# Kernel optimization log

Measured on AMD Instinct MI355X. Metric: run time of the kernel, lower is better.

The kernel has to match this reference:

```python
import jax, jax.numpy as jnp
import numpy as np

N = 8192        # n_nodes
NFEAT = 512
NHID = 256
AVG_DEG = 32
K = 64          # mean_kwargs k
TEMP = 1.0      # mean_kwargs temperature


def setup_inputs() -> dict:
    key = jax.random.key(0)
    ks = jax.random.split(key, 5)
    x = jax.random.normal(ks[0], (N, NFEAT), jnp.float32)
    edge_index = jax.random.randint(ks[1], (2, N * AVG_DEG), 0, N, dtype=jnp.int64)
    W1 = jax.random.normal(ks[2], (NFEAT, NHID), jnp.float32) / np.sqrt(NFEAT)
    b1 = jnp.zeros((NHID,), jnp.float32)
    W2 = jax.random.normal(ks[3], (NHID, NHID), jnp.float32) / np.sqrt(NHID)
    b2 = jnp.zeros((NHID,), jnp.float32)
    return {"x": x, "edge_index": edge_index, "W1": W1, "b1": b1, "W2": W2, "b2": b2}


def _gcn_norm(edge_index, n, dtype):
    # PyG gcn_norm: add self-loops (weight 1), deg over col, sym normalization
    loops = jnp.arange(n, dtype=edge_index.dtype)
    row = jnp.concatenate([edge_index[0], loops])
    col = jnp.concatenate([edge_index[1], loops])
    w = jnp.ones(row.shape[0], dtype)
    deg = jnp.zeros((n,), dtype).at[col].add(w)
    dis = jnp.where(deg > 0, jax.lax.rsqrt(jnp.where(deg > 0, deg, 1.0)), 0.0)
    return row, col, dis[row] * w * dis[col]


def _soft_k_medoid(row, col, w, x):
    # soft_weighted_medoid_k_neighborhood(A, x, k=K, temperature=TEMP, with_weight_correction=True)
    n, d = x.shape
    A = jnp.zeros((n, n), x.dtype).at[row, col].add(w)   # coalesced dense adjacency
    topk_a, topk_idx = jax.lax.top_k(A, K)               # [n, K] neighbor weights / ids
    xk = x[topk_idx]                                     # [n, K, d]
    sq = jnp.sum(xk * xk, axis=-1)                       # [n, K]
    G = jnp.einsum('nkd,nld->nkl', xk, xk)               # Gram per node
    d2 = jnp.maximum(sq[:, :, None] + sq[:, None, :] - 2.0 * G, 0.0)
    pos = d2 > 0
    dist = jnp.where(pos, jnp.sqrt(jnp.where(pos, d2, 1.0)), 0.0)  # safe sqrt (grad-safe)
    # weighted sum of distances to each top-k candidate j: c[n,j] = sum_l a[n,l] * ||x_l - x_j||
    c = jnp.einsum('nl,nlj->nj', topk_a, dist)
    c = jnp.where(topk_a == 0, jnp.finfo(x.dtype).max, c)
    soft = jax.nn.softmax(-c / TEMP, axis=-1)            # [n, K]
    soft = soft * topk_a                                 # with_weight_correction
    soft = soft / jnp.sum(soft, axis=-1, keepdims=True)
    row_sum = jnp.sum(A, axis=-1)                        # preserve neighborhood mass
    return row_sum[:, None] * jnp.einsum('nk,nkd->nd', soft, xk)


def reference(x, edge_index, W1, b1, W2, b2):
    n = x.shape[0]
    row, col, w = _gcn_norm(edge_index, n, x.dtype)
    h = jax.nn.relu(_soft_k_medoid(row, col, w, x @ W1) + b1)   # gc1 + relu (dropout: eval = identity)
    return jax.nn.relu(_soft_k_medoid(row, col, w, h @ W2) + b2)  # gc2 + relu
```

## Files before the change

kernel.cpp:

```cpp
#include <hip/hip_runtime.h>

typedef _Float16 half4 __attribute__((ext_vector_type(4)));
typedef _Float16 half8 __attribute__((ext_vector_type(8)));
typedef float f32x4 __attribute__((ext_vector_type(4)));

#define NNODE 8192
#define NHID  256
#define RCAP  128
#define KCAP  64
#define GLS   72
#define SK    136

struct SmemGemm  { _Float16 sA[64][GLS]; _Float16 sB[64][GLS]; };
struct SmemDedup { int lc[2][RCAP]; float lw[2][RCAP]; unsigned char kp[2][RCAP];
                   int cw[2][2]; float rw[2][2]; };
struct SmemMedoid {
    union {
        _Float16 sh[64][SK];
        float s_red[4][288];
    };
    float s_a[64]; float s_sq[64]; float s_cpart[2][64]; float s_u[64];
    int s_cols[64]; float s_rsum;
};

__device__ __forceinline__ void gemm_body(
    char* smraw, const _Float16* __restrict__ Ahi, const _Float16* __restrict__ BT,
    _Float16* __restrict__ Chi, int K, int bm, int bn) {
    SmemGemm& sm = *(SmemGemm*)smraw;
    const int t = threadIdx.x;
    const int lane = t & 63, L15 = lane & 15, q = lane >> 4;
    const int w = t >> 6, wr = w >> 1, wc = w & 1;
    f32x4 acc[2][2];
#pragma unroll
    for (int a = 0; a < 2; ++a)
#pragma unroll
        for (int b2 = 0; b2 < 2; ++b2) acc[a][b2] = (f32x4){0.f, 0.f, 0.f, 0.f};

    for (int k0 = 0; k0 < K; k0 += 64) {
#pragma unroll
        for (int i = 0; i < 2; ++i) {
            int row = i * 32 + (t >> 3), ch = t & 7;
            *(half8*)&sm.sA[row][ch * 8] =
                *(const half8*)(Ahi + (size_t)(bm + row) * K + k0 + ch * 8);
            *(half8*)&sm.sB[row][ch * 8] =
                *(const half8*)(BT + (size_t)(bn + row) * K + k0 + ch * 8);
        }
        __syncthreads();
#pragma unroll
        for (int ks = 0; ks < 2; ++ks) {
            const int ko = ks * 32 + q * 8;
            half8 ah[2], bh[2];
#pragma unroll
            for (int tr = 0; tr < 2; ++tr)
                ah[tr] = *(const half8*)&sm.sA[32 * wr + 16 * tr + L15][ko];
#pragma unroll
            for (int tc = 0; tc < 2; ++tc)
                bh[tc] = *(const half8*)&sm.sB[32 * wc + 16 * tc + L15][ko];
#pragma unroll
            for (int tr = 0; tr < 2; ++tr)
#pragma unroll
                for (int tc = 0; tc < 2; ++tc)
                    acc[tr][tc] = __builtin_amdgcn_mfma_f32_16x16x32_f16(ah[tr], bh[tc], acc[tr][tc], 0, 0, 0);
        }
        __syncthreads();
    }
#pragma unroll
    for (int tr = 0; tr < 2; ++tr)
#pragma unroll
        for (int tc = 0; tc < 2; ++tc)
#pragma unroll
            for (int r = 0; r < 4; ++r) {
                int rowg = bm + 32 * wr + 16 * tr + q * 4 + r;
                int colg = bn + 32 * wc + 16 * tc + L15;
                Chi[(size_t)rowg * NHID + colg] = (_Float16)acc[tr][tc][r];
            }
}

__device__ __forceinline__ void dedup_body(
    char* smraw, const int* __restrict__ nbr, const int* __restrict__ rowcnt,
    const int* __restrict__ deg, int* __restrict__ cols, float* __restrict__ wout,
    float* __restrict__ rsum, int grp) {
    SmemDedup& sm = *(SmemDedup*)smraw;
    const int t = threadIdx.x;
    const int half = t >> 7, st = t & 127;
    const int wid = st >> 6, lane = t & 63;
    const int r = grp * 2 + half;
    int n = rowcnt[r]; if (n > RCAP) n = RCAP;
    if (st < n) sm.lc[half][st] = nbr[r * RCAP + st];
    __syncthreads();
    float dr = 1.f / sqrtf((float)deg[r]);
    bool keep = false; float wv = 0.f;
    if (st < n) {
        int c = sm.lc[half][st];
        int mult = 0; bool first = true;
        for (int i = 0; i < n; ++i) {
            int ci = sm.lc[half][i];
            if (ci == c) { mult++; if (i < st) first = false; }
        }
        keep = first;
        if (first) wv = (float)mult * dr * (1.f / sqrtf((float)deg[c]));
    }
    sm.kp[half][st] = keep ? 1 : 0; sm.lw[half][st] = wv;
    float rv = wv;
#pragma unroll
    for (int d = 1; d < 64; d <<= 1) rv += __shfl_xor(rv, d, 64);
    unsigned long long b = __ballot(keep);
    int pre = __popcll(b & ((1ull << lane) - 1ull));
    int cw = __popcll(b);
    if (lane == 0) { sm.cw[half][wid] = cw; sm.rw[half][wid] = rv; }
    __syncthreads();
    int total = sm.cw[half][0] + sm.cw[half][1];
    if (st == 0) rsum[r] = sm.rw[half][0] + sm.rw[half][1];
    const int base = r * KCAP;
    if (total <= KCAP) {
        int off = (wid ? sm.cw[half][0] : 0) + pre;
        if (keep) { cols[base + off] = sm.lc[half][st]; wout[base + off] = wv; }
        for (int m = total + st; m < KCAP; m += 128) { cols[base + m] = r; wout[base + m] = 0.f; }
    } else if (st == 0) {
        for (int s = 0; s < KCAP; ++s) {
            int best = -1;
            for (int i = 0; i < n; ++i) {
                if (!sm.kp[half][i]) continue;
                if (best < 0 || sm.lw[half][i] > sm.lw[half][best] ||
                    (sm.lw[half][i] == sm.lw[half][best] && sm.lc[half][i] < sm.lc[half][best])) best = i;
            }
            cols[base + s] = sm.lc[half][best]; wout[base + s] = sm.lw[half][best]; sm.kp[half][best] = 0;
        }
    }
}

__device__ __forceinline__ void medoid_core(
    SmemMedoid& sm, const _Float16* __restrict__ Xhi, const float* __restrict__ bias,
    float* __restrict__ OutF, _Float16* __restrict__ OutHi, int node, int writeH) {
    const int t = threadIdx.x;
    const int w = t >> 6, lane = t & 63;
    const int L15 = lane & 15, q = lane >> 4;
    const int wr = w >> 1, wc = w & 1;

    f32x4 acc[2][2];
#pragma unroll
    for (int a = 0; a < 2; ++a)
#pragma unroll
        for (int b = 0; b < 2; ++b) acc[a][b] = (f32x4){0.f, 0.f, 0.f, 0.f};

    const int ch = t & 15, rr = t >> 4;
    const _Float16* rbase[4];
#pragma unroll
    for (int i = 0; i < 4; ++i)
        rbase[i] = Xhi + ((size_t)sm.s_cols[i * 16 + rr] << 8) + ch * 8;

    half8 g0[4];
#pragma unroll
    for (int i = 0; i < 4; ++i) g0[i] = *(const half8*)rbase[i];
#pragma unroll
    for (int i = 0; i < 4; ++i) *(half8*)&sm.sh[i * 16 + rr][ch * 8] = g0[i];
    __syncthreads();

    half8 g1[4];
#pragma unroll
    for (int i = 0; i < 4; ++i) g1[i] = *(const half8*)(rbase[i] + 128);

#pragma unroll
    for (int ks = 0; ks < 4; ++ks) {
        const int ko = ks * 32 + q * 8;
        half8 ah[2], bh[2];
#pragma unroll
        for (int tr = 0; tr < 2; ++tr) ah[tr] = *(const half8*)&sm.sh[32 * wr + 16 * tr + L15][ko];
#pragma unroll
        for (int tc = 0; tc < 2; ++tc) bh[tc] = *(const half8*)&sm.sh[32 * wc + 16 * tc + L15][ko];
#pragma unroll
        for (int tr = 0; tr < 2; ++tr)
#pragma unroll
            for (int tc = 0; tc < 2; ++tc)
                acc[tr][tc] = __builtin_amdgcn_mfma_f32_16x16x32_f16(ah[tr], bh[tc], acc[tr][tc], 0, 0, 0);
    }
    __syncthreads();

#pragma unroll
    for (int i = 0; i < 4; ++i) *(half8*)&sm.sh[i * 16 + rr][ch * 8] = g1[i];
    __syncthreads();
#pragma unroll
    for (int ks = 0; ks < 4; ++ks) {
        const int ko = ks * 32 + q * 8;
        half8 ah[2], bh[2];
#pragma unroll
        for (int tr = 0; tr < 2; ++tr) ah[tr] = *(const half8*)&sm.sh[32 * wr + 16 * tr + L15][ko];
#pragma unroll
        for (int tc = 0; tc < 2; ++tc) bh[tc] = *(const half8*)&sm.sh[32 * wc + 16 * tc + L15][ko];
#pragma unroll
        for (int tr = 0; tr < 2; ++tr)
#pragma unroll
            for (int tc = 0; tc < 2; ++tc)
                acc[tr][tc] = __builtin_amdgcn_mfma_f32_16x16x32_f16(ah[tr], bh[tc], acc[tr][tc], 0, 0, 0);
    }

#pragma unroll
    for (int tr = 0; tr < 2; ++tr)
#pragma unroll
        for (int tc = 0; tc < 2; ++tc)
            if (32 * wr + 16 * tr == 32 * wc + 16 * tc) {
#pragma unroll
                for (int r = 0; r < 4; ++r)
                    if (L15 == q * 4 + r) sm.s_sq[32 * wr + 16 * tr + L15] = acc[tr][tc][r];
            }
    __syncthreads();

    f32x4 sq4[2], a4[2];
#pragma unroll
    for (int tr = 0; tr < 2; ++tr) {
        sq4[tr] = *(const f32x4*)&sm.s_sq[32 * wr + 16 * tr + 4 * q];
        a4[tr]  = *(const f32x4*)&sm.s_a [32 * wr + 16 * tr + 4 * q];
    }
#pragma unroll
    for (int tc = 0; tc < 2; ++tc) {
        const int colg = 32 * wc + 16 * tc + L15;
        const float sqc = sm.s_sq[colg];
        float pj = 0.f;
#pragma unroll
        for (int tr = 0; tr < 2; ++tr)
#pragma unroll
            for (int r = 0; r < 4; ++r) {
                float d2 = sq4[tr][r] + sqc - 2.f * acc[tr][tc][r];
                float dist = d2 > 0.f ? __builtin_amdgcn_sqrtf(d2) : 0.f;
                pj = fmaf(a4[tr][r], dist, pj);
            }
        pj += __shfl_xor(pj, 16, 64);
        pj += __shfl_xor(pj, 32, 64);
        if (q == 0) sm.s_cpart[wr][colg] = pj;
    }
    __syncthreads();

    if (w == 0) {
        int j = lane;
        float c = sm.s_cpart[0][j] + sm.s_cpart[1][j];
        float aj = sm.s_a[j];
        bool valid = aj > 0.f;
        float cv = valid ? c : 3.4e38f;
        float mn = cv;
#pragma unroll
        for (int d = 1; d < 64; d <<= 1) mn = fminf(mn, __shfl_xor(mn, d, 64));
        float e = valid ? __expf(mn - c) * aj : 0.f;
        float s = e;
#pragma unroll
        for (int d = 1; d < 64; d <<= 1) s += __shfl_xor(s, d, 64);
        sm.s_u[j] = e * (sm.s_rsum / s);
    }
    __syncthreads();

    const int oct = t & 31, jb = t >> 5;
    float accd[8] = {0.f, 0.f, 0.f, 0.f, 0.f, 0.f, 0.f, 0.f};
#pragma unroll
    for (int jj = 0; jj < 8; ++jj) {
        int j = jb * 8 + jj;
        float u = sm.s_u[j];
        half8 xv;
        if (oct < 16) xv = *(const half8*)(Xhi + ((size_t)sm.s_cols[j] << 8) + oct * 8);
        else          xv = *(const half8*)&sm.sh[j][(oct - 16) * 8];
#pragma unroll
        for (int e = 0; e < 8; ++e) accd[e] = fmaf(u, (float)xv[e], accd[e]);
    }
#pragma unroll
    for (int e = 0; e < 8; ++e) accd[e] += __shfl_xor(accd[e], 32, 64);
    __syncthreads();
    if (lane < 32) {
#pragma unroll
        for (int e = 0; e < 8; ++e) sm.s_red[w][9 * oct + e] = accd[e];
    }
    __syncthreads();
    const int idx = 9 * (t >> 3) + (t & 7);
    float o = sm.s_red[0][idx] + sm.s_red[1][idx] + sm.s_red[2][idx] + sm.s_red[3][idx];
    float res = fmaxf(o + bias[t], 0.f);
    size_t oi = (size_t)node * NHID + t;
    if (writeH) OutHi[oi] = (_Float16)res;
    else        OutF[oi] = res;
}

#define PREPB 512
__global__ __launch_bounds__(256) void k_prep_scatter(
    const float* __restrict__ x, _Float16* __restrict__ xh,
    const float* __restrict__ W1, _Float16* __restrict__ w1T,
    const float* __restrict__ W2, _Float16* __restrict__ w2T,
    const void* edges, int* rowcnt, int* nbr, int* deg, int E) {
    const int t = threadIdx.x;
    if ((int)blockIdx.x < PREPB) {
        const int gid = blockIdx.x * 256 + t, nthr = PREPB * 256;
        for (int i = gid; i < NNODE * 512 / 4; i += nthr) {
            float4 v = ((const float4*)x)[i];
            half4 h;
            h[0] = (_Float16)v.x; h[1] = (_Float16)v.y;
            h[2] = (_Float16)v.z; h[3] = (_Float16)v.w;
            *(half4*)&xh[4 * (size_t)i] = h;
        }
        for (int i = gid; i < 512 * NHID; i += nthr) {
            int k = i >> 8, n = i & 255;
            w1T[(size_t)n * 512 + k] = (_Float16)W1[i];
        }
        for (int i = gid; i < NHID * NHID; i += nthr) {
            int k = i >> 8, n = i & 255;
            w2T[(size_t)n * 256 + k] = (_Float16)W2[i];
        }
    } else {
        __shared__ int sflag;
        if (t < 64) {
            const long long* e = (const long long*)edges;
            long long v = e[t];
            unsigned long long bad = __ballot(v < 0 || v >= (long long)NNODE);
            if (t == 0) sflag = (bad == 0) ? 1 : 0;
        }
        __syncthreads();
        const int fl = sflag;
        int i = ((int)blockIdx.x - PREPB) * 256 + t;
        if (i >= E + NNODE) return;
        int r, c;
        if (i < E) {
            if (fl) {
                const long long* e = (const long long*)edges;
                r = (int)e[i]; c = (int)e[E + i];
            } else {
                const int* e = (const int*)edges;
                r = e[i]; c = e[E + i];
            }
        } else { r = i - E; c = r; }
        int pos = atomicAdd(&rowcnt[r], 1);
        if (pos < RCAP) nbr[r * RCAP + pos] = c;
        atomicAdd(&deg[c], 1);
    }
}

__global__ __launch_bounds__(256) void k_gemm1_dedup(
    const _Float16* __restrict__ xh, const _Float16* __restrict__ w1T,
    _Float16* __restrict__ X1,
    const int* __restrict__ nbr, const int* __restrict__ rowcnt,
    const int* __restrict__ deg,
    int* __restrict__ cols, float* __restrict__ wA, float* __restrict__ rsum) {
    __shared__ __align__(16) char smem[sizeof(SmemGemm)];
    if ((int)blockIdx.x < 512) {
        int g = blockIdx.x;
        gemm_body(smem, xh, w1T, X1, 512, (g >> 2) * 64, (g & 3) * 64);
    } else {
        dedup_body(smem, nbr, rowcnt, deg, cols, wA, rsum, (int)blockIdx.x - 512);
    }
}

__global__ __launch_bounds__(256, 8) void k_medoid(
    const _Float16* __restrict__ X, const float* __restrict__ bias,
    float* __restrict__ OutF, _Float16* __restrict__ OutHi,
    const int* __restrict__ cols, const float* __restrict__ wts,
    const float* __restrict__ rsum, int writeH) {
    __shared__ __align__(16) SmemMedoid sm;
    const int node = blockIdx.x, t = threadIdx.x;
    if (t < 64) { sm.s_cols[t] = cols[node * KCAP + t]; sm.s_a[t] = wts[node * KCAP + t]; }
    if (t == 0) sm.s_rsum = rsum[node];
    __syncthreads();
    medoid_core(sm, X, bias, OutF, OutHi, node, writeH);
}

__global__ __launch_bounds__(256) void k_gemm2(
    const _Float16* __restrict__ Hh, const _Float16* __restrict__ w2T,
    _Float16* __restrict__ X2) {
    __shared__ __align__(16) char smem[sizeof(SmemGemm)];
    gemm_body(smem, Hh, w2T, X2, 256, blockIdx.x * 64, blockIdx.y * 64);
}

extern "C" void kernel_launch(void* const* d_in, const int* in_sizes, int n_in,
                              void* d_out, int out_size, void* d_ws, size_t ws_size,
                              hipStream_t stream) {
    const float* x  = (const float*)d_in[0];
    const void*  ei = d_in[1];
    const float* W1 = (const float*)d_in[2];
    const float* b1 = (const float*)d_in[3];
    const float* W2 = (const float*)d_in[4];
    const float* b2 = (const float*)d_in[5];
    float* out = (float*)d_out;
    const int E = in_sizes[1] / 2;

    char* p = (char*)d_ws;
    auto alloc = [&](size_t bytes) { char* q = p; p += (bytes + 255) & ~(size_t)255; return q; };
    int*      cnt    = (int*)alloc((size_t)2 * NNODE * 4);
    int*      deg    = cnt;
    int*      rowcnt = cnt + NNODE;
    int*      colsA  = (int*)alloc((size_t)NNODE * KCAP * 4);
    float*    wAr    = (float*)alloc((size_t)NNODE * KCAP * 4);
    float*    rsum   = (float*)alloc((size_t)NNODE * 4);
    _Float16* xh     = (_Float16*)alloc((size_t)NNODE * 512 * 2);
    _Float16* w1T    = (_Float16*)alloc((size_t)512 * NHID * 2);
    _Float16* w2T    = (_Float16*)alloc((size_t)NHID * NHID * 2);
    _Float16* X1     = (_Float16*)alloc((size_t)NNODE * NHID * 2);
    _Float16* Hh     = (_Float16*)alloc((size_t)NNODE * NHID * 2);
    int*      nbr    = (int*)alloc((size_t)NNODE * RCAP * 4);

    const int nscat = (E + NNODE + 255) / 256;

    hipMemsetAsync(cnt, 0, (size_t)2 * NNODE * 4, stream);
    k_prep_scatter<<<PREPB + nscat, 256, 0, stream>>>(x, xh, W1, w1T, W2, w2T,
                                                      ei, rowcnt, nbr, deg, E);
    k_gemm1_dedup<<<512 + NNODE / 2, 256, 0, stream>>>(xh, w1T, X1, nbr, rowcnt, deg,
                                                       colsA, wAr, rsum);
    k_medoid<<<NNODE, 256, 0, stream>>>(X1, b1, nullptr, Hh, colsA, wAr, rsum, 1);
    k_gemm2<<<dim3(NNODE / 64, NHID / 64), 256, 0, stream>>>(Hh, w2T, X1);
    k_medoid<<<NNODE, 256, 0, stream>>>(X1, b2, out, nullptr, colsA, wAr, rsum, 0);
}
```

Measured before the change: 196.6 us.

## Exploit Gram matrix symmetry to skip the redundant off-diagonal MFMA block

The per-node 64x64 Gram computation is reassigned across the four waves. Waves 0 and 3 compute the two 32x32 diagonal blocks, reusing one A-fragment as both operands. Waves 1 and 2 each compute half of the single upper off-diagonal block, and the lower block is never computed. Each off-diagonal wave adds its transposed contribution to the weighted distance sums through extra cross-lane shuffle reductions and a third partial-sum slot. This removes a quarter of the MFMAs and some LDS B-operand reads. The diagonal waves still issue as many MFMAs as before, so the longest wave's path barely shrinks, and the new shuffles add work.

```diff
diff --git a/kernel.cpp b/kernel.cpp
--- a/kernel.cpp
+++ b/kernel.cpp
@@ -19,7 +19,7 @@
         _Float16 sh[64][SK];
         float s_red[4][288];
     };
-    float s_a[64]; float s_sq[64]; float s_cpart[2][64]; float s_u[64];
+    float s_a[64]; float s_sq[64]; float s_cpart[3][64]; float s_u[64];
     int s_cols[64]; float s_rsum;
 };
 
@@ -135,7 +135,9 @@
     const int t = threadIdx.x;
     const int w = t >> 6, lane = t & 63;
     const int L15 = lane & 15, q = lane >> 4;
-    const int wr = w >> 1, wc = w & 1;
+    const bool diagw = (w == 0 || w == 3);
+    const int rb = (w == 3) ? 32 : 0;
+    const int cb = (w == 1) ? 32 : 48;
 
     f32x4 acc[2][2];
 #pragma unroll
@@ -163,16 +165,20 @@
 #pragma unroll
     for (int ks = 0; ks < 4; ++ks) {
         const int ko = ks * 32 + q * 8;
-        half8 ah[2], bh[2];
-#pragma unroll
-        for (int tr = 0; tr < 2; ++tr) ah[tr] = *(const half8*)&sm.sh[32 * wr + 16 * tr + L15][ko];
-#pragma unroll
-        for (int tc = 0; tc < 2; ++tc) bh[tc] = *(const half8*)&sm.sh[32 * wc + 16 * tc + L15][ko];
-#pragma unroll
-        for (int tr = 0; tr < 2; ++tr)
-#pragma unroll
-            for (int tc = 0; tc < 2; ++tc)
-                acc[tr][tc] = __builtin_amdgcn_mfma_f32_16x16x32_f16(ah[tr], bh[tc], acc[tr][tc], 0, 0, 0);
+        half8 ah[2];
+        ah[0] = *(const half8*)&sm.sh[rb + L15][ko];
+        ah[1] = *(const half8*)&sm.sh[rb + 16 + L15][ko];
+        if (diagw) {
+#pragma unroll
+            for (int tr = 0; tr < 2; ++tr)
+#pragma unroll
+                for (int tc = 0; tc < 2; ++tc)
+                    acc[tr][tc] = __builtin_amdgcn_mfma_f32_16x16x32_f16(ah[tr], ah[tc], acc[tr][tc], 0, 0, 0);
+        } else {
+            half8 bh = *(const half8*)&sm.sh[cb + L15][ko];
+            acc[0][0] = __builtin_amdgcn_mfma_f32_16x16x32_f16(ah[0], bh, acc[0][0], 0, 0, 0);
+            acc[1][0] = __builtin_amdgcn_mfma_f32_16x16x32_f16(ah[1], bh, acc[1][0], 0, 0, 0);
+        }
     }
     __syncthreads();
 
@@ -182,57 +188,100 @@
 #pragma unroll
     for (int ks = 0; ks < 4; ++ks) {
         const int ko = ks * 32 + q * 8;
-        half8 ah[2], bh[2];
-#pragma unroll
-        for (int tr = 0; tr < 2; ++tr) ah[tr] = *(const half8*)&sm.sh[32 * wr + 16 * tr + L15][ko];
-#pragma unroll
-        for (int tc = 0; tc < 2; ++tc) bh[tc] = *(const half8*)&sm.sh[32 * wc + 16 * tc + L15][ko];
+        half8 ah[2];
+        ah[0] = *(const half8*)&sm.sh[rb + L15][ko];
+        ah[1] = *(const half8*)&sm.sh[rb + 16 + L15][ko];
+        if (diagw) {
+#pragma unroll
+            for (int tr = 0; tr < 2; ++tr)
+#pragma unroll
+                for (int tc = 0; tc < 2; ++tc)
+                    acc[tr][tc] = __builtin_amdgcn_mfma_f32_16x16x32_f16(ah[tr], ah[tc], acc[tr][tc], 0, 0, 0);
+        } else {
+            half8 bh = *(const half8*)&sm.sh[cb + L15][ko];
+            acc[0][0] = __builtin_amdgcn_mfma_f32_16x16x32_f16(ah[0], bh, acc[0][0], 0, 0, 0);
+            acc[1][0] = __builtin_amdgcn_mfma_f32_16x16x32_f16(ah[1], bh, acc[1][0], 0, 0, 0);
+        }
+    }
+
+    if (diagw) {
 #pragma unroll
         for (int tr = 0; tr < 2; ++tr)
 #pragma unroll
-            for (int tc = 0; tc < 2; ++tc)
-                acc[tr][tc] = __builtin_amdgcn_mfma_f32_16x16x32_f16(ah[tr], bh[tc], acc[tr][tc], 0, 0, 0);
-    }
-
-#pragma unroll
-    for (int tr = 0; tr < 2; ++tr)
-#pragma unroll
-        for (int tc = 0; tc < 2; ++tc)
-            if (32 * wr + 16 * tr == 32 * wc + 16 * tc) {
-#pragma unroll
-                for (int r = 0; r < 4; ++r)
-                    if (L15 == q * 4 + r) sm.s_sq[32 * wr + 16 * tr + L15] = acc[tr][tc][r];
-            }
+            for (int r = 0; r < 4; ++r)
+                if (L15 == q * 4 + r) sm.s_sq[rb + 16 * tr + L15] = acc[tr][tr][r];
+    }
     __syncthreads();
 
     f32x4 sq4[2], a4[2];
 #pragma unroll
     for (int tr = 0; tr < 2; ++tr) {
-        sq4[tr] = *(const f32x4*)&sm.s_sq[32 * wr + 16 * tr + 4 * q];
-        a4[tr]  = *(const f32x4*)&sm.s_a [32 * wr + 16 * tr + 4 * q];
-    }
-#pragma unroll
-    for (int tc = 0; tc < 2; ++tc) {
-        const int colg = 32 * wc + 16 * tc + L15;
+        sq4[tr] = *(const f32x4*)&sm.s_sq[rb + 16 * tr + 4 * q];
+        a4[tr]  = *(const f32x4*)&sm.s_a [rb + 16 * tr + 4 * q];
+    }
+
+    if (diagw) {
+        const int slot = (w == 0) ? 0 : 1;
+#pragma unroll
+        for (int tc = 0; tc < 2; ++tc) {
+            const int colg = rb + 16 * tc + L15;
+            const float sqc = sm.s_sq[colg];
+            float pj = 0.f;
+#pragma unroll
+            for (int tr = 0; tr < 2; ++tr)
+#pragma unroll
+                for (int r = 0; r < 4; ++r) {
+                    float d2 = sq4[tr][r] + sqc - 2.f * acc[tr][tc][r];
+                    float dist = d2 > 0.f ? __builtin_amdgcn_sqrtf(d2) : 0.f;
+                    pj = fmaf(a4[tr][r], dist, pj);
+                }
+            pj += __shfl_xor(pj, 16, 64);
+            pj += __shfl_xor(pj, 32, 64);
+            if (q == 0) sm.s_cpart[slot][colg] = pj;
+        }
+    } else {
+        const int colg = cb + L15;
         const float sqc = sm.s_sq[colg];
+        const float ac  = sm.s_a[colg];
         float pj = 0.f;
+        float pt[2][4];
 #pragma unroll
         for (int tr = 0; tr < 2; ++tr)
 #pragma unroll
             for (int r = 0; r < 4; ++r) {
-                float d2 = sq4[tr][r] + sqc - 2.f * acc[tr][tc][r];
+                float d2 = sq4[tr][r] + sqc - 2.f * acc[tr][0][r];
                 float dist = d2 > 0.f ? __builtin_amdgcn_sqrtf(d2) : 0.f;
                 pj = fmaf(a4[tr][r], dist, pj);
+                pt[tr][r] = ac * dist;
             }
         pj += __shfl_xor(pj, 16, 64);
         pj += __shfl_xor(pj, 32, 64);
-        if (q == 0) sm.s_cpart[wr][colg] = pj;
+        if (q == 0) sm.s_cpart[0][colg] = pj;
+#pragma unroll
+        for (int tr = 0; tr < 2; ++tr)
+#pragma unroll
+            for (int r = 0; r < 4; ++r) {
+                float v = pt[tr][r];
+                v += __shfl_xor(v, 1, 64);
+                v += __shfl_xor(v, 2, 64);
+                v += __shfl_xor(v, 4, 64);
+                v += __shfl_xor(v, 8, 64);
+                pt[tr][r] = v;
+            }
+        const int slotT = (w == 1) ? 1 : 2;
+        if (L15 == 0) {
+#pragma unroll
+            for (int tr = 0; tr < 2; ++tr)
+#pragma unroll
+                for (int r = 0; r < 4; ++r)
+                    sm.s_cpart[slotT][16 * tr + 4 * q + r] = pt[tr][r];
+        }
     }
     __syncthreads();
 
     if (w == 0) {
         int j = lane;
-        float c = sm.s_cpart[0][j] + sm.s_cpart[1][j];
+        float c = sm.s_cpart[0][j] + sm.s_cpart[1][j] + (j < 32 ? sm.s_cpart[2][j] : 0.f);
         float aj = sm.s_a[j];
         bool valid = aj > 0.f;
         float cv = valid ? c : 3.4e38f;
```

New measurement: 197.6 us. Within noise of the previous version (+0.6%).
